# Kernel optimization log

Measured on AMD Instinct MI355X. Metric: run time of the kernel, lower is better.

The kernel has to match this reference:

```python
import jax, jax.numpy as jnp
import numpy as np

D_MODEL, D_FF, N_EXPERTS, TOP_K = 1024, 4096, 4, 2
B, S = 4, 2048


def setup_inputs() -> dict:
    key = jax.random.key(0)
    ks = jax.random.split(key, 7)
    s_r = 1.0 / np.sqrt(D_MODEL)
    s_f = 1.0 / np.sqrt(D_FF)
    return {
        "x": jax.random.normal(ks[0], (B, S, D_MODEL), dtype=jnp.float32),
        "Wr": jax.random.uniform(ks[1], (D_MODEL, N_EXPERTS), jnp.float32, -s_r, s_r),
        "br": jnp.zeros((N_EXPERTS,), jnp.float32),
        "W1": jax.random.uniform(ks[2], (N_EXPERTS, D_MODEL, D_FF), jnp.float32, -s_r, s_r),
        "b1": jax.random.uniform(ks[3], (N_EXPERTS, D_FF), jnp.float32, -s_r, s_r),
        "W2": jax.random.uniform(ks[4], (N_EXPERTS, D_FF, D_MODEL), jnp.float32, -s_f, s_f),
        "b2": jax.random.uniform(ks[5], (N_EXPERTS, D_MODEL), jnp.float32, -s_f, s_f),
    }


def reference(x, Wr, br, W1, b1, W2, b2):
    # Router: (B,S,E)
    router_logits = jnp.einsum("bsd,de->bse", x, Wr) + br
    router_probs = jax.nn.softmax(router_logits, axis=-1)
    top_k_probs, top_k_idx = jax.lax.top_k(router_probs, TOP_K)  # (B,S,K)
    top_k_probs = top_k_probs / jnp.sum(top_k_probs, axis=-1, keepdims=True)

    # Dense all-experts compute (faithful to original module).
    h = jnp.einsum("bsd,edf->bsef", x, W1) + b1          # (B,S,E,F)
    h = jax.nn.gelu(h, approximate=False)                 # torch nn.GELU (erf)
    expert_out = jnp.einsum("bsef,efd->bsed", h, W2) + b2  # (B,S,E,D)

    # Gather top-k expert outputs and combine with renormalized probs.
    sel = jnp.take_along_axis(expert_out, top_k_idx[..., None], axis=2)  # (B,S,K,D)
    out = jnp.sum(sel * top_k_probs[..., None], axis=2)   # (B,S,D)
    return out
```

## Files before the change

kernel.cpp:

```cpp
#include <hip/hip_runtime.h>
#include <hip/hip_bf16.h>
#include <hip/hip_fp16.h>
#include <stdint.h>

typedef float    f32x4 __attribute__((ext_vector_type(4)));
typedef float    fvec4 __attribute__((ext_vector_type(4)));
typedef _Float16 f16x8 __attribute__((ext_vector_type(8)));

#define D_MODEL 1024
#define D_FF    4096
#define NTOK    8192
#define CAP_ROWS 16896
#define NRB      132

#define OFF_W1  0UL
#define OFF_W2  33554432UL
#define OFF_XG  67108864UL
#define OFF_H   101711872UL
#define OFF_CNT 240123904UL
#define OFF_OFS 240123936UL
#define OFF_TOK 240124160UL
#define OFF_E12 240259328UL
#define OFF_W12 240292096UL
#define WS_NEED 240357632UL

__device__ __forceinline__ void gload_lds16(const void* g, void* l) {
  __builtin_amdgcn_global_load_lds(
      (const __attribute__((address_space(1))) unsigned int*)g,
      (__attribute__((address_space(3))) unsigned int*)l, 16, 0, 0);
}

__device__ __forceinline__ float fast_gelu(float v) {
  float v2 = v * v;
  float y2 = v * (2.302118131f + 0.10293924f * v2);
  float t = exp2f(y2);
  return v - v * __builtin_amdgcn_rcpf(1.f + t);
}

__device__ __forceinline__ void wtrans_body(
    const float* __restrict__ in, _Float16* __restrict__ out,
    int K, int N, int e, int n0, int k0, float (*tile)[65]) {
  const float* src = in + (size_t)e * K * N;
  _Float16* dst = out + (size_t)e * K * N;
  int t = threadIdx.x;
  {
    int kk = t >> 2, nc = (t & 3) * 16;
    const float* p = src + (size_t)(k0 + kk) * N + n0 + nc;
#pragma unroll
    for (int j = 0; j < 4; ++j) {
      fvec4 v = *(const fvec4*)(p + j * 4);
      tile[kk][nc + j * 4 + 0] = v[0]; tile[kk][nc + j * 4 + 1] = v[1];
      tile[kk][nc + j * 4 + 2] = v[2]; tile[kk][nc + j * 4 + 3] = v[3];
    }
  }
  __syncthreads();
  {
    int nn = t >> 2, kb = (t & 3) * 16;
    f16x8 o0, o1;
#pragma unroll
    for (int j = 0; j < 8; ++j) o0[j] = (_Float16)tile[kb + j][nn];
#pragma unroll
    for (int j = 0; j < 8; ++j) o1[j] = (_Float16)tile[kb + 8 + j][nn];
    _Float16* q = dst + (size_t)(n0 + nn) * K + k0 + kb;
    *(f16x8*)q = o0;
    *((f16x8*)q + 1) = o1;
  }
}

__global__ __launch_bounds__(256) void rwc_k(
    const float* __restrict__ x, const float* __restrict__ Wr,
    const float* __restrict__ br, int* __restrict__ e12,
    float* __restrict__ w12,
    const float* __restrict__ W1, _Float16* __restrict__ W1f,
    _Float16* __restrict__ x16) {
  __shared__ float tile[64][65];
  int b = blockIdx.x;
  if (b >= 6144) {
    int row = (b - 6144) * 2 + (threadIdx.x >> 7);
    int tid = threadIdx.x & 127;
    const float* src = x + (size_t)row * D_MODEL + tid * 8;
    fvec4 v0 = *(const fvec4*)src;
    fvec4 v1 = *(const fvec4*)(src + 4);
    f16x8 o;
#pragma unroll
    for (int j = 0; j < 4; ++j) { o[j] = (_Float16)v0[j]; o[4 + j] = (_Float16)v1[j]; }
    *(f16x8*)(x16 + (size_t)row * D_MODEL + tid * 8) = o;
    return;
  }
  if (b >= 2048) {
    int bb = b - 2048;
    int n0 = (bb & 63) * 64, k0 = ((bb >> 6) & 15) * 64, e = bb >> 10;
    wtrans_body(W1, W1f, 1024, 4096, e, n0, k0, tile);
    return;
  }
  int wid = threadIdx.x >> 6, lane = threadIdx.x & 63;
  int t = b * 4 + wid;
  const float* xr = x + (size_t)t * D_MODEL;
  float a0 = 0.f, a1 = 0.f, a2 = 0.f, a3 = 0.f;
#pragma unroll
  for (int c = 0; c < 4; ++c) {
    int d0 = c * 256 + lane * 4;
    fvec4 xv = *(const fvec4*)(xr + d0);
#pragma unroll
    for (int j = 0; j < 4; ++j) {
      fvec4 wv = *(const fvec4*)(Wr + (size_t)(d0 + j) * 4);
      a0 += xv[j] * wv[0]; a1 += xv[j] * wv[1];
      a2 += xv[j] * wv[2]; a3 += xv[j] * wv[3];
    }
  }
#pragma unroll
  for (int m = 32; m; m >>= 1) {
    a0 += __shfl_xor(a0, m, 64); a1 += __shfl_xor(a1, m, 64);
    a2 += __shfl_xor(a2, m, 64); a3 += __shfl_xor(a3, m, 64);
  }
  if (lane == 0) {
    float l[4] = {a0 + br[0], a1 + br[1], a2 + br[2], a3 + br[3]};
    int e1 = 0; float m1 = l[0];
#pragma unroll
    for (int e = 1; e < 4; ++e) if (l[e] > m1) { m1 = l[e]; e1 = e; }
    int e2 = -1; float m2 = -1e30f;
#pragma unroll
    for (int e = 0; e < 4; ++e) if (e != e1 && l[e] > m2) { m2 = l[e]; e2 = e; }
    float tt = expf(m2 - m1);
    float w1 = 1.f / (1.f + tt), w2 = tt / (1.f + tt);
    e12[t] = e1 | (e2 << 8);
    w12[2 * t] = w1; w12[2 * t + 1] = w2;
  }
}

__global__ __launch_bounds__(256) void plan_k(
    int* __restrict__ e12, const float* __restrict__ w12,
    int* __restrict__ counts, int* __restrict__ offs,
    int* __restrict__ tok) {
  __shared__ int ls[4][256];
  __shared__ int lt[4];
  __shared__ int lo[5];
  int tid = threadIdx.x;
  int t0 = tid * 32;
  int pe[32];
  int c0 = 0, c1 = 0, c2 = 0, c3 = 0;
#pragma unroll
  for (int j = 0; j < 32; ++j) {
    int p = e12[t0 + j];
    pe[j] = p;
    int e1 = p & 255, e2 = p >> 8;
    c0 += (e1 == 0) + (e2 == 0);
    c1 += (e1 == 1) + (e2 == 1);
    c2 += (e1 == 2) + (e2 == 2);
    c3 += (e1 == 3) + (e2 == 3);
  }
  ls[0][tid] = c0; ls[1][tid] = c1; ls[2][tid] = c2; ls[3][tid] = c3;
  __syncthreads();
  int wv = tid >> 6, lane = tid & 63;
  {
    int s0 = ls[wv][lane * 4 + 0], s1 = ls[wv][lane * 4 + 1];
    int s2 = ls[wv][lane * 4 + 2], s3 = ls[wv][lane * 4 + 3];
    int s = s0 + s1 + s2 + s3;
    int incl = s;
#pragma unroll
    for (int d = 1; d < 64; d <<= 1) {
      int tsh = __shfl_up(incl, d, 64);
      if (lane >= d) incl += tsh;
    }
    int excl = incl - s;
    ls[wv][lane * 4 + 0] = excl;
    ls[wv][lane * 4 + 1] = excl + s0;
    ls[wv][lane * 4 + 2] = excl + s0 + s1;
    ls[wv][lane * 4 + 3] = excl + s0 + s1 + s2;
    if (lane == 63) lt[wv] = incl;
  }
  __syncthreads();
  if (tid == 0) {
    int o = 0;
#pragma unroll
    for (int e = 0; e < 4; ++e) {
      lo[e] = o; offs[e] = o; counts[e] = lt[e];
      o += (lt[e] + 127) & ~127;
    }
    lo[4] = o; offs[4] = o;
  }
  __syncthreads();
  int b0 = lo[0] + ls[0][tid], b1 = lo[1] + ls[1][tid];
  int b2 = lo[2] + ls[2][tid], b3 = lo[3] + ls[3][tid];
#pragma unroll
  for (int j = 0; j < 32; ++j) {
    int p = pe[j];
    int t = t0 + j;
    int e1 = p & 255, e2 = p >> 8;
    int s1 = (e1 == 0) ? b0 : (e1 == 1) ? b1 : (e1 == 2) ? b2 : b3;
    tok[s1] = t;
    b0 += (e1 == 0); b1 += (e1 == 1); b2 += (e1 == 2); b3 += (e1 == 3);
    int s2 = (e2 == 0) ? b0 : (e2 == 1) ? b1 : (e2 == 2) ? b2 : b3;
    tok[s2] = t;
    b0 += (e2 == 0); b1 += (e2 == 1); b2 += (e2 == 2); b3 += (e2 == 3);
    e12[t] = s1 | (s2 << 16);
  }
#pragma unroll
  for (int e = 0; e < 4; ++e) {
    int start = lo[e] + lt[e];
    int end = lo[e + 1];
    for (int i = start + tid; i < end; i += 256) tok[i] = 0;
  }
}

__device__ __forceinline__ f16x8 lds_frag(const char* base, int row, int kbyte) {
  return *(const f16x8*)(base + row * 128 + (kbyte ^ ((row & 7) << 4)));
}

__global__ __launch_bounds__(256, 2) void gemm1x_k(
    const _Float16* __restrict__ x16, const _Float16* __restrict__ B,
    const float* __restrict__ bias, const int* __restrict__ offs,
    const int* __restrict__ counts, const int* __restrict__ tok,
    _Float16* __restrict__ outH,
    const float* __restrict__ W2, _Float16* __restrict__ W2f) {
  __shared__ char lds[49152];
  int bid = blockIdx.x;
  if (bid >= 2112) {
    int bb = bid - 2112;
    int n0 = (bb & 15) * 64, k0 = ((bb >> 4) & 63) * 64, e = bb >> 10;
    wtrans_body(W2, W2f, 4096, 1024, e, n0, k0, (float(*)[65])lds);
    return;
  }
  int wg = (bid & 7) * 264 + (bid >> 3);
  int col = wg & 15, row = wg >> 4;
  int rowBase = row * 128;
  if (rowBase >= offs[4]) return;
  int e = 0;
  while (e < 3 && rowBase >= offs[e + 1]) ++e;
  if (rowBase >= offs[e] + counts[e]) return;
  int colBase = col * 256;

  int tid = threadIdx.x, wid = tid >> 6, lane = tid & 63;
  int wr = wid >> 1, wc = wid & 1;
  int ln = lane & 15;
  int srow = lane >> 3;
  int kx = (lane & 7) ^ srow;
  const _Float16* Asrc[4];
#pragma unroll
  for (int i = 0; i < 4; ++i) {
    int tk = tok[rowBase + (wid * 4 + i) * 8 + srow];
    Asrc[i] = x16 + (size_t)tk * 1024 + kx * 8;
  }
  const _Float16* Bbase = B + (size_t)e * D_FF * 1024 + (size_t)colBase * 1024 + kx * 8;
  char* ldsA = lds;
  char* ldsB = lds + 16384;

  f32x4 acc[4][8];
  f32x4 zero = {0.f, 0.f, 0.f, 0.f};
#pragma unroll
  for (int m = 0; m < 4; ++m)
#pragma unroll
    for (int n = 0; n < 8; ++n) acc[m][n] = zero;

  for (int k0 = 0; k0 < 1024; k0 += 64) {
#pragma unroll
    for (int i = 0; i < 4; ++i) {
      int chunk = wid * 4 + i;
      gload_lds16(Asrc[i] + k0, ldsA + chunk * 1024);
    }
#pragma unroll
    for (int i = 0; i < 8; ++i) {
      int chunk = wid * 8 + i;
      gload_lds16(Bbase + (size_t)(chunk * 8 + srow) * 1024 + k0, ldsB + chunk * 1024);
    }
    __syncthreads();
#pragma unroll
    for (int kk = 0; kk < 2; ++kk) {
      int kbyte = kk * 64 + (lane >> 4) * 16;
      f16x8 af[4], bf[8];
#pragma unroll
      for (int m = 0; m < 4; ++m)
        af[m] = lds_frag(ldsA, wr * 64 + m * 16 + ln, kbyte);
#pragma unroll
      for (int n = 0; n < 8; ++n)
        bf[n] = lds_frag(ldsB, wc * 128 + n * 16 + ln, kbyte);
#pragma unroll
      for (int m = 0; m < 4; ++m)
#pragma unroll
        for (int n = 0; n < 8; ++n)
          acc[m][n] = __builtin_amdgcn_mfma_f32_16x16x32_f16(af[m], bf[n], acc[m][n], 0, 0, 0);
    }
    __syncthreads();
  }

  int col0 = colBase + wc * 128 + ln;
  float bv[8];
#pragma unroll
  for (int n = 0; n < 8; ++n) bv[n] = bias[(size_t)e * D_FF + col0 + n * 16];
#pragma unroll
  for (int m = 0; m < 4; ++m) {
    int rbase = rowBase + wr * 64 + m * 16 + (lane >> 4) * 4;
#pragma unroll
    for (int j = 0; j < 4; ++j) {
      size_t ro = (size_t)(rbase + j) * D_FF;
#pragma unroll
      for (int n = 0; n < 8; ++n) {
        float v = fast_gelu(acc[m][n][j] + bv[n]);
        outH[ro + col0 + n * 16] = (_Float16)v;
      }
    }
  }
}

#define G2BAR  asm volatile("s_barrier" ::: "memory")
#define G2VM8  asm volatile("s_waitcnt vmcnt(8)" ::: "memory")
#define G2LGKM asm volatile("s_waitcnt lgkmcnt(0)" ::: "memory")

__global__ __launch_bounds__(256, 2) void gemm2_k(
    const _Float16* __restrict__ A, const _Float16* __restrict__ B,
    const float* __restrict__ bias, const int* __restrict__ offs,
    const int* __restrict__ counts, _Float16* __restrict__ Eout) {
  __shared__ char lds[65536];
  int bid = blockIdx.x;
  int wg = (bid & 7) * 132 + (bid >> 3);
  int col = wg & 7, row = wg >> 3;
  int rowBase = row * 128;
  if (rowBase >= offs[4]) return;
  int e = 0;
  while (e < 3 && rowBase >= offs[e + 1]) ++e;
  int eoff = offs[e], cnt = counts[e];
  if (rowBase >= eoff + cnt) return;
  int colBase = col * 128;

  int tid = threadIdx.x, wid = tid >> 6, lane = tid & 63;
  int wr = wid >> 1, wc = wid & 1;
  int ln = lane & 15;
  int srow = lane >> 3;
  int kx = (lane & 7) ^ srow;
  const _Float16* Abase = A + (size_t)rowBase * 4096 + kx * 8;
  const _Float16* Bbase = B + (size_t)e * D_MODEL * 4096 + (size_t)colBase * 4096 + kx * 8;

  f32x4 acc[4][4];
  f32x4 zero = {0.f, 0.f, 0.f, 0.f};
#pragma unroll
  for (int m = 0; m < 4; ++m)
#pragma unroll
    for (int n = 0; n < 4; ++n) acc[m][n] = zero;

  auto STAGE = [&](int kt, int b) {
    char* lA = lds + (b << 15);
    char* lB = lA + 16384;
    int k0 = kt * 64;
#pragma unroll
    for (int i = 0; i < 4; ++i) {
      int chunk = wid * 4 + i;
      gload_lds16(Abase + (size_t)(chunk * 8 + srow) * 4096 + k0, lA + chunk * 1024);
      gload_lds16(Bbase + (size_t)(chunk * 8 + srow) * 4096 + k0, lB + chunk * 1024);
    }
  };

  STAGE(0, 0);
  STAGE(1, 1);

  for (int t = 0; t < 64; ++t) {
    G2VM8;
    G2BAR;
    const char* cA = lds + ((t & 1) << 15);
    const char* cB = cA + 16384;
#pragma unroll
    for (int kk = 0; kk < 2; ++kk) {
      int kbyte = kk * 64 + (lane >> 4) * 16;
      f16x8 af[4], bf[4];
#pragma unroll
      for (int m = 0; m < 4; ++m)
        af[m] = lds_frag(cA, wr * 64 + m * 16 + ln, kbyte);
#pragma unroll
      for (int n = 0; n < 4; ++n)
        bf[n] = lds_frag(cB, wc * 64 + n * 16 + ln, kbyte);
      G2LGKM;
      __builtin_amdgcn_s_setprio(1);
#pragma unroll
      for (int m = 0; m < 4; ++m)
#pragma unroll
        for (int n = 0; n < 4; ++n)
          acc[m][n] = __builtin_amdgcn_mfma_f32_16x16x32_f16(af[m], bf[n], acc[m][n], 0, 0, 0);
      __builtin_amdgcn_s_setprio(0);
    }
    G2BAR;
    int tn = t + 2; if (tn > 63) tn = 63;
    STAGE(tn, t & 1);
  }
  asm volatile("s_waitcnt vmcnt(0)" ::: "memory");

  int col0 = colBase + wc * 64 + ln;
  float bv[4];
#pragma unroll
  for (int n = 0; n < 4; ++n) bv[n] = bias[(size_t)e * D_MODEL + col0 + n * 16];
#pragma unroll
  for (int m = 0; m < 4; ++m) {
    int rbase = rowBase + wr * 64 + m * 16 + (lane >> 4) * 4;
#pragma unroll
    for (int j = 0; j < 4; ++j) {
      int grow = rbase + j;
      if (grow - eoff < cnt) {
        size_t o = (size_t)grow * D_MODEL + col0;
#pragma unroll
        for (int n = 0; n < 4; ++n)
          Eout[o + n * 16] = (_Float16)(acc[m][n][j] + bv[n]);
      }
    }
  }
}

__global__ __launch_bounds__(256) void combine_k(
    const _Float16* __restrict__ Eout, const int* __restrict__ sl12,
    const float* __restrict__ w12, float* __restrict__ out) {
  int t = blockIdx.x * 2 + (threadIdx.x >> 7);
  int tid = threadIdx.x & 127;
  int p = sl12[t];
  int s1 = p & 0xffff, s2 = (p >> 16) & 0xffff;
  float w1 = w12[2 * t], w2 = w12[2 * t + 1];
  f16x8 a = *(const f16x8*)(Eout + (size_t)s1 * D_MODEL + tid * 8);
  f16x8 b = *(const f16x8*)(Eout + (size_t)s2 * D_MODEL + tid * 8);
  fvec4 o0, o1;
#pragma unroll
  for (int j = 0; j < 4; ++j) {
    o0[j] = w1 * (float)a[j] + w2 * (float)b[j];
    o1[j] = w1 * (float)a[4 + j] + w2 * (float)b[4 + j];
  }
  float* dst = out + (size_t)t * D_MODEL + tid * 8;
  *(fvec4*)dst = o0;
  *(fvec4*)(dst + 4) = o1;
}

extern "C" void kernel_launch(void* const* d_in, const int* in_sizes, int n_in,
                              void* d_out, int out_size, void* d_ws, size_t ws_size,
                              hipStream_t stream) {
  const float* x  = (const float*)d_in[0];
  const float* Wr = (const float*)d_in[1];
  const float* br = (const float*)d_in[2];
  const float* W1 = (const float*)d_in[3];
  const float* b1 = (const float*)d_in[4];
  const float* W2 = (const float*)d_in[5];
  const float* b2 = (const float*)d_in[6];
  float* out = (float*)d_out;
  char* ws = (char*)d_ws;
  if (ws_size < WS_NEED) return;

  _Float16* W1f = (_Float16*)(ws + OFF_W1);
  _Float16* W2f = (_Float16*)(ws + OFF_W2);
  _Float16* x16 = (_Float16*)(ws + OFF_XG);
  _Float16* H   = (_Float16*)(ws + OFF_H);
  int*   counts = (int*)(ws + OFF_CNT);
  int*   offs   = (int*)(ws + OFF_OFS);
  int*   tok    = (int*)(ws + OFF_TOK);
  int*   e12    = (int*)(ws + OFF_E12);
  float* w12    = (float*)(ws + OFF_W12);
  _Float16* Eout = x16;

  rwc_k<<<10240, 256, 0, stream>>>(x, Wr, br, e12, w12, W1, W1f, x16);
  plan_k<<<1, 256, 0, stream>>>(e12, w12, counts, offs, tok);
  gemm1x_k<<<6208, 256, 0, stream>>>(x16, W1f, b1, offs, counts, tok, H, W2, W2f);
  gemm2_k<<<NRB * 8, 256, 0, stream>>>(H, W2f, b2, offs, counts, Eout);
  combine_k<<<NTOK / 2, 256, 0, stream>>>(Eout, e12, w12, out);
}
```

Measured before the change: 439.2 us.

## Double-buffer gemm1 with 512-thread blocks and software-pipelined global-to-LDS loads

```diff
diff --git a/kernel.cpp b/kernel.cpp
--- a/kernel.cpp
+++ b/kernel.cpp
@@ -39,10 +39,9 @@
 
 __device__ __forceinline__ void wtrans_body(
     const float* __restrict__ in, _Float16* __restrict__ out,
-    int K, int N, int e, int n0, int k0, float (*tile)[65]) {
+    int K, int N, int e, int n0, int k0, int t, float (*tile)[65]) {
   const float* src = in + (size_t)e * K * N;
   _Float16* dst = out + (size_t)e * K * N;
-  int t = threadIdx.x;
   {
     int kk = t >> 2, nc = (t & 3) * 16;
     const float* p = src + (size_t)(k0 + kk) * N + n0 + nc;
@@ -65,6 +64,7 @@
     *(f16x8*)q = o0;
     *((f16x8*)q + 1) = o1;
   }
+  __syncthreads();
 }
 
 __global__ __launch_bounds__(256) void rwc_k(
@@ -90,7 +90,7 @@
   if (b >= 2048) {
     int bb = b - 2048;
     int n0 = (bb & 63) * 64, k0 = ((bb >> 6) & 15) * 64, e = bb >> 10;
-    wtrans_body(W1, W1f, 1024, 4096, e, n0, k0, tile);
+    wtrans_body(W1, W1f, 1024, 4096, e, n0, k0, threadIdx.x, tile);
     return;
   }
   int wid = threadIdx.x >> 6, lane = threadIdx.x & 63;
@@ -207,18 +207,31 @@
   return *(const f16x8*)(base + row * 128 + (kbyte ^ ((row & 7) << 4)));
 }
 
-__global__ __launch_bounds__(256, 2) void gemm1x_k(
+#define GVM6   asm volatile("s_waitcnt vmcnt(6)" ::: "memory")
+#define GVM8   asm volatile("s_waitcnt vmcnt(8)" ::: "memory")
+#define GVM0   asm volatile("s_waitcnt vmcnt(0)" ::: "memory")
+#define GBAR   asm volatile("s_barrier" ::: "memory")
+#define GLGKM  asm volatile("s_waitcnt lgkmcnt(0)" ::: "memory")
+
+__global__ __launch_bounds__(512) void gemm1x_k(
     const _Float16* __restrict__ x16, const _Float16* __restrict__ B,
     const float* __restrict__ bias, const int* __restrict__ offs,
     const int* __restrict__ counts, const int* __restrict__ tok,
     _Float16* __restrict__ outH,
     const float* __restrict__ W2, _Float16* __restrict__ W2f) {
-  __shared__ char lds[49152];
+  extern __shared__ char smem[];
   int bid = blockIdx.x;
   if (bid >= 2112) {
-    int bb = bid - 2112;
-    int n0 = (bb & 15) * 64, k0 = ((bb >> 4) & 63) * 64, e = bb >> 10;
-    wtrans_body(W2, W2f, 4096, 1024, e, n0, k0, (float(*)[65])lds);
+    int half = threadIdx.x >> 8;
+    int t = threadIdx.x & 255;
+    float (*tile)[65] = (float(*)[65])(smem + half * 16640);
+    int base = (bid - 2112) * 4 + half * 2;
+#pragma unroll
+    for (int rep = 0; rep < 2; ++rep) {
+      int T = base + rep;
+      int n0 = (T & 15) * 64, k0 = ((T >> 4) & 63) * 64, e = T >> 10;
+      wtrans_body(W2, W2f, 4096, 1024, e, n0, k0, t, tile);
+    }
     return;
   }
   int wg = (bid & 7) * 264 + (bid >> 3);
@@ -231,62 +244,76 @@
   int colBase = col * 256;
 
   int tid = threadIdx.x, wid = tid >> 6, lane = tid & 63;
-  int wr = wid >> 1, wc = wid & 1;
+  int wr = wid >> 2, wc = wid & 3;
   int ln = lane & 15;
   int srow = lane >> 3;
   int kx = (lane & 7) ^ srow;
-  const _Float16* Asrc[4];
-#pragma unroll
-  for (int i = 0; i < 4; ++i) {
-    int tk = tok[rowBase + (wid * 4 + i) * 8 + srow];
+  const _Float16* Asrc[2];
+#pragma unroll
+  for (int i = 0; i < 2; ++i) {
+    int tk = tok[rowBase + (wid * 2 + i) * 8 + srow];
     Asrc[i] = x16 + (size_t)tk * 1024 + kx * 8;
   }
   const _Float16* Bbase = B + (size_t)e * D_FF * 1024 + (size_t)colBase * 1024 + kx * 8;
-  char* ldsA = lds;
-  char* ldsB = lds + 16384;
-
-  f32x4 acc[4][8];
+
+  f32x4 acc[4][4];
   f32x4 zero = {0.f, 0.f, 0.f, 0.f};
 #pragma unroll
   for (int m = 0; m < 4; ++m)
 #pragma unroll
-    for (int n = 0; n < 8; ++n) acc[m][n] = zero;
-
-  for (int k0 = 0; k0 < 1024; k0 += 64) {
+    for (int n = 0; n < 4; ++n) acc[m][n] = zero;
+
+  auto STAGE = [&](int kt, int b) {
+    char* lA = smem + b * 49152;
+    char* lB = lA + 16384;
+    int k0 = kt * 64;
+#pragma unroll
+    for (int i = 0; i < 2; ++i)
+      gload_lds16(Asrc[i] + k0, lA + (wid * 2 + i) * 1024);
 #pragma unroll
     for (int i = 0; i < 4; ++i) {
       int chunk = wid * 4 + i;
-      gload_lds16(Asrc[i] + k0, ldsA + chunk * 1024);
-    }
-#pragma unroll
-    for (int i = 0; i < 8; ++i) {
-      int chunk = wid * 8 + i;
-      gload_lds16(Bbase + (size_t)(chunk * 8 + srow) * 1024 + k0, ldsB + chunk * 1024);
-    }
-    __syncthreads();
+      gload_lds16(Bbase + (size_t)(chunk * 8 + srow) * 1024 + k0, lB + chunk * 1024);
+    }
+  };
+
+  STAGE(0, 0);
+  STAGE(1, 1);
+
+  for (int t = 0; t < 16; ++t) {
+    GVM6;
+    GBAR;
+    const char* cA = smem + (t & 1) * 49152;
+    const char* cB = cA + 16384;
 #pragma unroll
     for (int kk = 0; kk < 2; ++kk) {
       int kbyte = kk * 64 + (lane >> 4) * 16;
-      f16x8 af[4], bf[8];
+      f16x8 af[4], bf[4];
 #pragma unroll
       for (int m = 0; m < 4; ++m)
-        af[m] = lds_frag(ldsA, wr * 64 + m * 16 + ln, kbyte);
-#pragma unroll
-      for (int n = 0; n < 8; ++n)
-        bf[n] = lds_frag(ldsB, wc * 128 + n * 16 + ln, kbyte);
+        af[m] = lds_frag(cA, wr * 64 + m * 16 + ln, kbyte);
+#pragma unroll
+      for (int n = 0; n < 4; ++n)
+        bf[n] = lds_frag(cB, wc * 64 + n * 16 + ln, kbyte);
+      GLGKM;
+      __builtin_amdgcn_s_setprio(1);
 #pragma unroll
       for (int m = 0; m < 4; ++m)
 #pragma unroll
-        for (int n = 0; n < 8; ++n)
+        for (int n = 0; n < 4; ++n)
           acc[m][n] = __builtin_amdgcn_mfma_f32_16x16x32_f16(af[m], bf[n], acc[m][n], 0, 0, 0);
-    }
-    __syncthreads();
-  }
-
-  int col0 = colBase + wc * 128 + ln;
-  float bv[8];
-#pragma unroll
-  for (int n = 0; n < 8; ++n) bv[n] = bias[(size_t)e * D_FF + col0 + n * 16];
+      __builtin_amdgcn_s_setprio(0);
+    }
+    GBAR;
+    int tn = t + 2; if (tn > 15) tn = 15;
+    STAGE(tn, t & 1);
+  }
+  GVM0;
+
+  int col0 = colBase + wc * 64 + ln;
+  float bv[4];
+#pragma unroll
+  for (int n = 0; n < 4; ++n) bv[n] = bias[(size_t)e * D_FF + col0 + n * 16];
 #pragma unroll
   for (int m = 0; m < 4; ++m) {
     int rbase = rowBase + wr * 64 + m * 16 + (lane >> 4) * 4;
@@ -294,17 +321,13 @@
     for (int j = 0; j < 4; ++j) {
       size_t ro = (size_t)(rbase + j) * D_FF;
 #pragma unroll
-      for (int n = 0; n < 8; ++n) {
+      for (int n = 0; n < 4; ++n) {
         float v = fast_gelu(acc[m][n][j] + bv[n]);
         outH[ro + col0 + n * 16] = (_Float16)v;
       }
     }
   }
 }
-
-#define G2BAR  asm volatile("s_barrier" ::: "memory")
-#define G2VM8  asm volatile("s_waitcnt vmcnt(8)" ::: "memory")
-#define G2LGKM asm volatile("s_waitcnt lgkmcnt(0)" ::: "memory")
 
 __global__ __launch_bounds__(256, 2) void gemm2_k(
     const _Float16* __restrict__ A, const _Float16* __restrict__ B,
@@ -353,8 +376,8 @@
   STAGE(1, 1);
 
   for (int t = 0; t < 64; ++t) {
-    G2VM8;
-    G2BAR;
+    GVM8;
+    GBAR;
     const char* cA = lds + ((t & 1) << 15);
     const char* cB = cA + 16384;
 #pragma unroll
@@ -367,7 +390,7 @@
 #pragma unroll
       for (int n = 0; n < 4; ++n)
         bf[n] = lds_frag(cB, wc * 64 + n * 16 + ln, kbyte);
-      G2LGKM;
+      GLGKM;
       __builtin_amdgcn_s_setprio(1);
 #pragma unroll
       for (int m = 0; m < 4; ++m)
@@ -376,11 +399,11 @@
           acc[m][n] = __builtin_amdgcn_mfma_f32_16x16x32_f16(af[m], bf[n], acc[m][n], 0, 0, 0);
       __builtin_amdgcn_s_setprio(0);
     }
-    G2BAR;
+    GBAR;
     int tn = t + 2; if (tn > 63) tn = 63;
     STAGE(tn, t & 1);
   }
-  asm volatile("s_waitcnt vmcnt(0)" ::: "memory");
+  GVM0;
 
   int col0 = colBase + wc * 64 + ln;
   float bv[4];
@@ -448,9 +471,12 @@
   float* w12    = (float*)(ws + OFF_W12);
   _Float16* Eout = x16;
 
+  hipFuncSetAttribute((const void*)gemm1x_k,
+                      hipFuncAttributeMaxDynamicSharedMemorySize, 98304);
+
   rwc_k<<<10240, 256, 0, stream>>>(x, Wr, br, e12, w12, W1, W1f, x16);
   plan_k<<<1, 256, 0, stream>>>(e12, w12, counts, offs, tok);
-  gemm1x_k<<<6208, 256, 0, stream>>>(x16, W1f, b1, offs, counts, tok, H, W2, W2f);
+  gemm1x_k<<<3136, 512, 98304, stream>>>(x16, W1f, b1, offs, counts, tok, H, W2, W2f);
   gemm2_k<<<NRB * 8, 256, 0, stream>>>(H, W2f, b2, offs, counts, Eout);
   combine_k<<<NTOK / 2, 256, 0, stream>>>(Eout, e12, w12, out);
 }
```

Result: slower. 477.2 us (+8.7%).
